# Performance work log

Measured on AMD Instinct MI355X. Metric: run time of the kernel, lower is better.

Reference implementation:

```python
import jax, jax.numpy as jnp
import numpy as np

L = 3
ALPHA = 1.0
BETA = 1.0
SCALING = 3.0
N_NODES = 100000
N_EDGES = 1250000
D_FEAT = 64


def spmm(row, col, w, z, n):
    # out[i] = sum_{e: row_e == i} w_e * z[col_e]  (torch_sparse.matmul reduce='sum')
    return jax.ops.segment_sum(z[col] * w[:, None], row, num_segments=n)


def setup_inputs() -> dict:
    key = jax.random.key(0)
    k1, k2, k3, k4 = jax.random.split(key, 4)
    x = jax.random.normal(k1, (N_NODES, D_FEAT), dtype=jnp.float32)
    edge_index = jax.random.randint(k2, (2, N_EDGES), 0, N_NODES, dtype=jnp.int64)
    # surrogate for symmetric-normalized adjacency weights
    edge_weight = jax.random.uniform(k3, (N_EDGES,), dtype=jnp.float32) * 0.2
    gammas = jnp.full((L + 1, 1), min(1.0 / SCALING, 1.0), dtype=jnp.float32)
    return {"x": x, "edge_index": edge_index, "edge_weight": edge_weight, "gammas": gammas}


def reference(x, edge_index, edge_weight, gammas):
    n = x.shape[0]
    row, col = edge_index[0], edge_index[1]
    a, b = ALPHA, BETA

    zs = [x]  # z_0 = x
    # l = 1: c * z0 + (a+b+2)/2 * A z0
    z1 = ((a - b) / 2) * zs[-1] + ((a + b + 2) / 2) * spmm(row, col, edge_weight, zs[-1], n)
    zs.append(z1)
    for l in range(2, L + 1):
        c0 = 2 * l * (l + a + b) * (2 * l + a + b - 2)
        c1 = (2 * l + a + b - 1) * (a ** 2 - b ** 2)
        c2 = (2 * l + a + b - 1) * (2 * l + a + b) * (2 * l + a + b - 2)
        c3 = 2 * (l + a - 1) * (l + b - 1) * (2 * l + a + b)
        Az = spmm(row, col, edge_weight, zs[-1], n)
        z = (c1 * zs[-1] + c2 * Az - c3 * zs[-2]) / c0
        zs.append(z)

    coefs = jnp.cumprod(jnp.tanh(gammas) * SCALING, axis=0)  # [L+1, 1]
    Z = jnp.stack(zs, axis=1)  # [N, L+1, d]
    return (Z * coefs).mean(axis=1)
```

## Files before the change

### kernel.cpp

```cpp
#include <hip/hip_runtime.h>
#include <hip/hip_fp16.h>
#include <math.h>

#define D 64
#define RB_SHIFT 6
#define RB 64
#define CAP 1024
#define CAPE 2048
#define MAX_NB 1600
#define LDSE 2048


__global__ void bin_scatter_kernel(const int* __restrict__ row, const int* __restrict__ col,
                                   const float* __restrict__ w,
                                   int* __restrict__ cursor,
                                   int2* __restrict__ binned, int E, int NB) {
    __shared__ int lbase[MAX_NB];
    __shared__ int lcur[MAX_NB];
    int chunk = (E + gridDim.x - 1) / gridDim.x;
    int lo = blockIdx.x * chunk;
    int hi = min(E, lo + chunk);
    for (int j = threadIdx.x; j < NB; j += blockDim.x) { lbase[j] = 0; lcur[j] = 0; }
    __syncthreads();
    for (int i = lo + threadIdx.x; i < hi; i += blockDim.x)
        atomicAdd(&lbase[row[i] >> RB_SHIFT], 1);
    __syncthreads();
    for (int j = threadIdx.x; j < NB; j += blockDim.x) {
        int c = lbase[j];
        int base = c ? atomicAdd(&cursor[j], c) : 0;
        lbase[j] = j * CAP + base;
    }
    __syncthreads();
    for (int i = lo + threadIdx.x; i < hi; i += blockDim.x) {
        int r = row[i];
        int b = r >> RB_SHIFT;
        int off = atomicAdd(&lcur[b], 1);
        binned[lbase[b] + off] = make_int2(col[i] | ((r & (RB - 1)) << 17), __float_as_int(w[i]));
    }
}

__global__ void bucket_sort_kernel(const int2* __restrict__ binned,
                                   const int* __restrict__ cursor,
                                   int2* __restrict__ edges, int2* __restrict__ rowinfo,
                                   int N, int NB) {
    __shared__ alignas(16) int2 perm[CAPE];
    __shared__ int hist[RB];
    __shared__ int plr[RB];
    __shared__ int scn[RB];
    __shared__ int pst[RB];
    __shared__ int cur[RB];
    int b = blockIdx.x, t = threadIdx.x;
    int base = b * CAP;
    int cnt = cursor[b];
    if (cnt > CAP) cnt = CAP;

    if (t < RB) hist[t] = 0;
    __syncthreads();
    for (int i = t; i < cnt; i += 256)
        atomicAdd(&hist[(binned[base + i].x >> 17) & (RB - 1)], 1);
    __syncthreads();
    if (t < RB) plr[t] = (hist[t] + 3) & ~3;
    __syncthreads();
    if (t < RB) {
        int qb = t & ~3;
        scn[t] = max(max(plr[qb], plr[qb | 1]), max(plr[qb | 2], plr[qb | 3]));
    }
    __syncthreads();
    for (int off = 1; off < RB; off <<= 1) {
        int v = (t < RB && t >= off) ? scn[t - off] : 0;
        __syncthreads();
        if (t < RB) scn[t] += v;
        __syncthreads();
    }
    if (t < RB) {
        int qb = t & ~3;
        int pl = max(max(plr[qb], plr[qb | 1]), max(plr[qb | 2], plr[qb | 3]));
        int ps = scn[t] - pl;
        pst[t] = ps;
        cur[t] = ps;
    }
    __syncthreads();
    for (int i = t; i < cnt; i += 256) {
        int2 e = binned[base + i];
        int rl = (e.x >> 17) & (RB - 1);
        int d = atomicAdd(&cur[rl], 1);
        __half2 wh2 = __half2half2(__float2half(__int_as_float(e.y)));
        perm[d] = make_int2((e.x & 0x1FFFF) << 7, *(int*)&wh2);
    }
    __syncthreads();
    if (t < RB) {
        int h = hist[t];
        int ps = pst[t];
        int qb = t & ~3;
        int pl = max(max(plr[qb], plr[qb | 1]), max(plr[qb | 2], plr[qb | 3]));
        int dummycol = (h > 0) ? perm[ps].x : 0;
        for (int i = h; i < pl; ++i) perm[ps + i] = make_int2(dummycol, 0);
        int r0 = b * RB + t;
        if (r0 < N) rowinfo[r0] = make_int2(b * CAPE + ps, pl);
    }
    __syncthreads();
    int ptotal = scn[RB - 1];
    if (ptotal > CAPE) ptotal = CAPE;
    int n4 = ptotal >> 1;
    const int4* ps4 = (const int4*)perm;
    int4* pd4 = (int4*)(edges + (size_t)b * CAPE);
    for (int i = t; i < n4; i += 256) pd4[i] = ps4[i];
}

__global__ void tohalf_kernel(const float4* __restrict__ in, ushort4* __restrict__ o, int n4) {
    int i = blockIdx.x * blockDim.x + threadIdx.x;
    int stride = gridDim.x * blockDim.x;
    for (; i < n4; i += stride) {
        float4 f = in[i];
        ushort4 h;
        h.x = __half_as_ushort(__float2half(f.x));
        h.y = __half_as_ushort(__float2half(f.y));
        h.z = __half_as_ushort(__float2half(f.z));
        h.w = __half_as_ushort(__float2half(f.w));
        o[i] = h;
    }
}

__device__ __forceinline__ void quad_row_acc_lds(const int2* __restrict__ lds_desc, int cnt,
                                                 const char* __restrict__ g2b, int boff,
                                                 __half2& acc0, __half2& acc1) {
    acc0 = __half2half2(__ushort_as_half((unsigned short)0));
    acc1 = acc0;
    for (int jb = 0; jb < cnt; jb += 4) {
        const int4* p4 = (const int4*)(lds_desc + jb);
        int4 d0 = p4[0];
        int4 d1 = p4[1];
        int2 g0 = *(const int2*)(g2b + (size_t)(unsigned)(d0.x + boff));
        int2 g1 = *(const int2*)(g2b + (size_t)(unsigned)(d0.z + boff));
        int2 g2 = *(const int2*)(g2b + (size_t)(unsigned)(d1.x + boff));
        int2 g3 = *(const int2*)(g2b + (size_t)(unsigned)(d1.z + boff));
        acc0 = __hfma2(*(__half2*)&d0.y, *(__half2*)&g0.x, acc0);
        acc1 = __hfma2(*(__half2*)&d0.y, *(__half2*)&g0.y, acc1);
        acc0 = __hfma2(*(__half2*)&d0.w, *(__half2*)&g1.x, acc0);
        acc1 = __hfma2(*(__half2*)&d0.w, *(__half2*)&g1.y, acc1);
        acc0 = __hfma2(*(__half2*)&d1.y, *(__half2*)&g2.x, acc0);
        acc1 = __hfma2(*(__half2*)&d1.y, *(__half2*)&g2.y, acc1);
        acc0 = __hfma2(*(__half2*)&d1.w, *(__half2*)&g3.x, acc0);
        acc1 = __hfma2(*(__half2*)&d1.w, *(__half2*)&g3.y, acc1);
    }
}

__global__ void spmm_z_kernel(const int2* __restrict__ rowinfo,
                              const int2* __restrict__ edges,
                              const __half2* __restrict__ gsrc2,
                              const __half2* __restrict__ zp2_2,
                              __half2* __restrict__ zdst2,
                              float cA, float cC, int N) {
    __shared__ alignas(16) int2 lds[LDSE];
    int t = threadIdx.x;
    int bid = blockIdx.x;
    int r0 = bid * 16;

    int gs = rowinfo[r0].x;
    int2 rlast = rowinfo[min(r0 + 15, N - 1)];
    int span = rlast.x + rlast.y - gs;
    if (span > LDSE) span = LDSE;
    {
        int n4 = span >> 1;
        const int4* s4 = (const int4*)(edges + gs);
        int4* d4 = (int4*)lds;
        for (int i = t; i < n4; i += 256) d4[i] = s4[i];
    }
    __syncthreads();

    int wv = t >> 6;
    int lane = t & 63;
    int q = lane >> 4;
    int k16 = lane & 15;
    int rr = r0 + wv * 4 + q;
    bool valid = rr < N;
    int r = valid ? rr : N - 1;

    int2 ri = rowinfo[r];
    int cnt = __builtin_amdgcn_readfirstlane(ri.y);
    int off = ri.x - gs;
    if (off < 0 || off + cnt > span) off = 0;

    int boff = k16 * 8;
    size_t rb = (size_t)r * 128 + boff;
    float2 p0 = make_float2(0.f, 0.f), p1 = p0;
    if (zp2_2) {
        int2 pz = *(const int2*)((const char*)zp2_2 + rb);
        p0 = __half22float2(*(__half2*)&pz.x);
        p1 = __half22float2(*(__half2*)&pz.y);
    }

    __half2 acc0, acc1;
    quad_row_acc_lds(lds + off, cnt, (const char*)gsrc2, boff, acc0, acc1);
    float2 a0 = __half22float2(acc0);
    float2 a1 = __half22float2(acc1);

    float2 z0 = make_float2(cA * a0.x, cA * a0.y);
    float2 z1 = make_float2(cA * a1.x, cA * a1.y);
    if (zp2_2) {
        z0.x = fmaf(cC, p0.x, z0.x); z0.y = fmaf(cC, p0.y, z0.y);
        z1.x = fmaf(cC, p1.x, z1.x); z1.y = fmaf(cC, p1.y, z1.y);
    }
    if (valid) {
        __half2 h0 = __floats2half2_rn(z0.x, z0.y);
        __half2 h1 = __floats2half2_rn(z1.x, z1.y);
        int2 st;
        st.x = *(int*)&h0;
        st.y = *(int*)&h1;
        *(int2*)((char*)zdst2 + rb) = st;
    }
}

__global__ void spmm_final_kernel(const int2* __restrict__ rowinfo,
                                  const int2* __restrict__ edges,
                                  const __half2* __restrict__ z2h2,
                                  const __half2* __restrict__ z1h2,
                                  const __half2* __restrict__ xh2,
                                  float* __restrict__ out,
                                  const float* __restrict__ gammas,
                                  float cA, float cC, int N) {
    __shared__ alignas(16) int2 lds[LDSE];
    int t = threadIdx.x;
    int bid = blockIdx.x;
    int r0 = bid * 16;

    int gs = rowinfo[r0].x;
    int2 rlast = rowinfo[min(r0 + 15, N - 1)];
    int span = rlast.x + rlast.y - gs;
    if (span > LDSE) span = LDSE;
    {
        int n4 = span >> 1;
        const int4* s4 = (const int4*)(edges + gs);
        int4* d4 = (int4*)lds;
        for (int i = t; i < n4; i += 256) d4[i] = s4[i];
    }
    __syncthreads();

    int wv = t >> 6;
    int lane = t & 63;
    int q = lane >> 4;
    int k16 = lane & 15;
    int rr = r0 + wv * 4 + q;
    bool valid = rr < N;
    int r = valid ? rr : N - 1;

    float t0 = tanhf(gammas[0]) * 3.0f;
    float t1 = t0 * (tanhf(gammas[1]) * 3.0f);
    float t2 = t1 * (tanhf(gammas[2]) * 3.0f);
    float t3 = t2 * (tanhf(gammas[3]) * 3.0f);

    int2 ri = rowinfo[r];
    int cnt = __builtin_amdgcn_readfirstlane(ri.y);
    int off = ri.x - gs;
    if (off < 0 || off + cnt > span) off = 0;

    int boff = k16 * 8;
    size_t rb = (size_t)r * 128 + boff;
    int2 pz1 = *(const int2*)((const char*)z1h2 + rb);
    int2 pz2 = *(const int2*)((const char*)z2h2 + rb);
    int2 pxv = *(const int2*)((const char*)xh2 + rb);

    __half2 acc0, acc1;
    quad_row_acc_lds(lds + off, cnt, (const char*)z2h2, boff, acc0, acc1);
    float2 a0 = __half22float2(acc0);
    float2 a1 = __half22float2(acc1);

    float2 z1v0 = __half22float2(*(__half2*)&pz1.x);
    float2 z1v1 = __half22float2(*(__half2*)&pz1.y);
    float2 z2v0 = __half22float2(*(__half2*)&pz2.x);
    float2 z2v1 = __half22float2(*(__half2*)&pz2.y);
    float2 xv0  = __half22float2(*(__half2*)&pxv.x);
    float2 xv1  = __half22float2(*(__half2*)&pxv.y);

    float2 z30 = make_float2(cA * a0.x + cC * z1v0.x, cA * a0.y + cC * z1v0.y);
    float2 z31 = make_float2(cA * a1.x + cC * z1v1.x, cA * a1.y + cC * z1v1.y);

    if (valid) {
        float4 o;
        o.x = 0.25f * (t0 * xv0.x + t1 * z1v0.x + t2 * z2v0.x + t3 * z30.x);
        o.y = 0.25f * (t0 * xv0.y + t1 * z1v0.y + t2 * z2v0.y + t3 * z30.y);
        o.z = 0.25f * (t0 * xv1.x + t1 * z1v1.x + t2 * z2v1.x + t3 * z31.x);
        o.w = 0.25f * (t0 * xv1.y + t1 * z1v1.y + t2 * z2v1.y + t3 * z31.y);
        ((float4*)out)[(size_t)r * 16 + k16] = o;
    }
}

extern "C" void kernel_launch(void* const* d_in, const int* in_sizes, int n_in,
                              void* d_out, int out_size, void* d_ws, size_t ws_size,
                              hipStream_t stream) {
    const float* x      = (const float*)d_in[0];
    const int*   ei     = (const int*)d_in[1];
    const float* w      = (const float*)d_in[2];
    const float* gammas = (const float*)d_in[3];

    const int E = in_sizes[1] / 2;
    const int N = in_sizes[0] / D;
    const long NF = (long)N * D;
    const int NB = (N + RB - 1) >> RB_SHIFT;

    float* out = (float*)d_out;

    char* p = (char*)d_ws;
    __half* xh  = (__half*)p;       p += NF * sizeof(__half);
    __half* z1h = (__half*)p;       p += NF * sizeof(__half);
    __half* z2h = (__half*)p;       p += NF * sizeof(__half);
    int* cursor = (int*)p;          p += NB * sizeof(int);
    p = (char*)(((uintptr_t)p + 15) & ~(uintptr_t)15);
    int2* rowinfo = (int2*)p;       p += (size_t)N * sizeof(int2);
    int2* binned = (int2*)p;        p += (size_t)NB * CAP * sizeof(int2);
    int2* edges = (int2*)p;

    const int* row = ei;
    const int* col = ei + E;

    const double a = 1.0, b = 1.0;
    const int blk = 256;

    hipMemsetAsync(cursor, 0, (size_t)NB * sizeof(int), stream);
    bin_scatter_kernel<<<256, 1024, 0, stream>>>(row, col, w, cursor, binned, E, NB);
    bucket_sort_kernel<<<NB, 256, 0, stream>>>(binned, cursor, edges, rowinfo, N, NB);
    tohalf_kernel<<<1024, blk, 0, stream>>>((const float4*)x, (ushort4*)xh, (int)(NF / 4));

    const int sgrid = (N + 15) / 16;

    {
        float cA = (float)((a + b + 2.0) / 2.0);
        spmm_z_kernel<<<sgrid, blk, 0, stream>>>(rowinfo, edges, (const __half2*)xh,
                                                 nullptr, (__half2*)z1h, cA, 0.0f, N);
    }

    {
        int l = 2;
        double c0 = 2.0 * l * (l + a + b) * (2.0 * l + a + b - 2.0);
        double c2 = (2.0 * l + a + b - 1.0) * (2.0 * l + a + b) * (2.0 * l + a + b - 2.0);
        double c3 = 2.0 * (l + a - 1.0) * (l + b - 1.0) * (2.0 * l + a + b);
        spmm_z_kernel<<<sgrid, blk, 0, stream>>>(rowinfo, edges, (const __half2*)z1h,
                                                 (const __half2*)xh, (__half2*)z2h,
                                                 (float)(c2 / c0), (float)(-c3 / c0), N);
    }

    {
        int l = 3;
        double c0 = 2.0 * l * (l + a + b) * (2.0 * l + a + b - 2.0);
        double c2 = (2.0 * l + a + b - 1.0) * (2.0 * l + a + b) * (2.0 * l + a + b - 2.0);
        double c3 = 2.0 * (l + a - 1.0) * (l + b - 1.0) * (2.0 * l + a + b);
        spmm_final_kernel<<<sgrid, blk, 0, stream>>>(rowinfo, edges, (const __half2*)z2h,
                                                     (const __half2*)z1h, (const __half2*)xh,
                                                     out, gammas,
                                                     (float)(c2 / c0), (float)(-c3 / c0), N);
    }
}
```

Before: 199.5 us.

## Replace bin-and-bucket-sort CSR build with row histogram, scan, and atomic scatter

The padded per-row edge layout used to be built in two stages: edges were binned into fixed-capacity buckets of 64 rows, then each bucket was sorted in shared memory and copied out. It is now built from a global per-row atomic histogram, a per-block scan that computes padded row offsets and fills pad slots, and a direct atomic scatter of edges into their final positions. This removes the intermediate binned buffer and the extra pass over it. In exchange it relies on two rounds of contended global atomics plus random 8-byte writes, and it adds a memset of a per-row counter array. Pad entries now point at column 0 with zero weight, and the order of edges within a row is no longer deterministic.

```diff
diff --git a/kernel.cpp b/kernel.cpp
--- a/kernel.cpp
+++ b/kernel.cpp
@@ -5,106 +5,85 @@
 #define D 64
 #define RB_SHIFT 6
 #define RB 64
-#define CAP 1024
 #define CAPE 2048
-#define MAX_NB 1600
 #define LDSE 2048
 
 
-__global__ void bin_scatter_kernel(const int* __restrict__ row, const int* __restrict__ col,
-                                   const float* __restrict__ w,
-                                   int* __restrict__ cursor,
-                                   int2* __restrict__ binned, int E, int NB) {
-    __shared__ int lbase[MAX_NB];
-    __shared__ int lcur[MAX_NB];
-    int chunk = (E + gridDim.x - 1) / gridDim.x;
-    int lo = blockIdx.x * chunk;
-    int hi = min(E, lo + chunk);
-    for (int j = threadIdx.x; j < NB; j += blockDim.x) { lbase[j] = 0; lcur[j] = 0; }
-    __syncthreads();
-    for (int i = lo + threadIdx.x; i < hi; i += blockDim.x)
-        atomicAdd(&lbase[row[i] >> RB_SHIFT], 1);
-    __syncthreads();
-    for (int j = threadIdx.x; j < NB; j += blockDim.x) {
-        int c = lbase[j];
-        int base = c ? atomicAdd(&cursor[j], c) : 0;
-        lbase[j] = j * CAP + base;
-    }
-    __syncthreads();
-    for (int i = lo + threadIdx.x; i < hi; i += blockDim.x) {
-        int r = row[i];
-        int b = r >> RB_SHIFT;
-        int off = atomicAdd(&lcur[b], 1);
-        binned[lbase[b] + off] = make_int2(col[i] | ((r & (RB - 1)) << 17), __float_as_int(w[i]));
-    }
-}
-
-__global__ void bucket_sort_kernel(const int2* __restrict__ binned,
-                                   const int* __restrict__ cursor,
-                                   int2* __restrict__ edges, int2* __restrict__ rowinfo,
-                                   int N, int NB) {
-    __shared__ alignas(16) int2 perm[CAPE];
-    __shared__ int hist[RB];
+__global__ void hist_kernel(const int* __restrict__ row, int* __restrict__ rowcnt, int E) {
+    int tid = blockIdx.x * blockDim.x + threadIdx.x;
+    int stride = gridDim.x * blockDim.x;
+    int n4 = E >> 2;
+    const int4* r4 = (const int4*)row;
+    for (int i = tid; i < n4; i += stride) {
+        int4 r = r4[i];
+        atomicAdd(&rowcnt[r.x], 1);
+        atomicAdd(&rowcnt[r.y], 1);
+        atomicAdd(&rowcnt[r.z], 1);
+        atomicAdd(&rowcnt[r.w], 1);
+    }
+    for (int i = (n4 << 2) + tid; i < E; i += stride)
+        atomicAdd(&rowcnt[row[i]], 1);
+}
+
+__global__ void scan_pad_kernel(const int* __restrict__ rowcnt,
+                                int2* __restrict__ edges,
+                                int2* __restrict__ rowinfo,
+                                int* __restrict__ curs, int N) {
     __shared__ int plr[RB];
     __shared__ int scn[RB];
-    __shared__ int pst[RB];
-    __shared__ int cur[RB];
     int b = blockIdx.x, t = threadIdx.x;
-    int base = b * CAP;
-    int cnt = cursor[b];
-    if (cnt > CAP) cnt = CAP;
-
-    if (t < RB) hist[t] = 0;
+    int r = b * RB + t;
+    int h = (r < N) ? rowcnt[r] : 0;
+    plr[t] = (h + 3) & ~3;
     __syncthreads();
-    for (int i = t; i < cnt; i += 256)
-        atomicAdd(&hist[(binned[base + i].x >> 17) & (RB - 1)], 1);
-    __syncthreads();
-    if (t < RB) plr[t] = (hist[t] + 3) & ~3;
-    __syncthreads();
-    if (t < RB) {
-        int qb = t & ~3;
-        scn[t] = max(max(plr[qb], plr[qb | 1]), max(plr[qb | 2], plr[qb | 3]));
-    }
+    int qb = t & ~3;
+    int pl = max(max(plr[qb], plr[qb | 1]), max(plr[qb | 2], plr[qb | 3]));
+    scn[t] = pl;
     __syncthreads();
     for (int off = 1; off < RB; off <<= 1) {
-        int v = (t < RB && t >= off) ? scn[t - off] : 0;
+        int v = (t >= off) ? scn[t - off] : 0;
         __syncthreads();
-        if (t < RB) scn[t] += v;
+        scn[t] += v;
         __syncthreads();
     }
-    if (t < RB) {
-        int qb = t & ~3;
-        int pl = max(max(plr[qb], plr[qb | 1]), max(plr[qb | 2], plr[qb | 3]));
-        int ps = scn[t] - pl;
-        pst[t] = ps;
-        cur[t] = ps;
-    }
-    __syncthreads();
-    for (int i = t; i < cnt; i += 256) {
-        int2 e = binned[base + i];
-        int rl = (e.x >> 17) & (RB - 1);
-        int d = atomicAdd(&cur[rl], 1);
-        __half2 wh2 = __half2half2(__float2half(__int_as_float(e.y)));
-        perm[d] = make_int2((e.x & 0x1FFFF) << 7, *(int*)&wh2);
-    }
-    __syncthreads();
-    if (t < RB) {
-        int h = hist[t];
-        int ps = pst[t];
-        int qb = t & ~3;
-        int pl = max(max(plr[qb], plr[qb | 1]), max(plr[qb | 2], plr[qb | 3]));
-        int dummycol = (h > 0) ? perm[ps].x : 0;
-        for (int i = h; i < pl; ++i) perm[ps + i] = make_int2(dummycol, 0);
-        int r0 = b * RB + t;
-        if (r0 < N) rowinfo[r0] = make_int2(b * CAPE + ps, pl);
-    }
-    __syncthreads();
-    int ptotal = scn[RB - 1];
-    if (ptotal > CAPE) ptotal = CAPE;
-    int n4 = ptotal >> 1;
-    const int4* ps4 = (const int4*)perm;
-    int4* pd4 = (int4*)(edges + (size_t)b * CAPE);
-    for (int i = t; i < n4; i += 256) pd4[i] = ps4[i];
+    int ps = scn[t] - pl;
+    if (ps + pl > CAPE) { ps = 0; pl = 0; h = 0; }
+    if (r < N) {
+        int start = b * CAPE + ps;
+        rowinfo[r] = make_int2(start, pl);
+        curs[r] = start;
+        for (int i = h; i < pl; ++i) edges[start + i] = make_int2(0, 0);
+    }
+}
+
+__global__ void scatter_kernel(const int* __restrict__ row, const int* __restrict__ col,
+                               const float* __restrict__ w,
+                               int* __restrict__ curs, int2* __restrict__ edges, int E) {
+    int tid = blockIdx.x * blockDim.x + threadIdx.x;
+    int stride = gridDim.x * blockDim.x;
+    int n4 = E >> 2;
+    const int4* r4 = (const int4*)row;
+    const int4* c4 = (const int4*)col;
+    const float4* w4 = (const float4*)w;
+    for (int i = tid; i < n4; i += stride) {
+        int4 rr = r4[i];
+        int4 cc = c4[i];
+        float4 ww = w4[i];
+        int rs[4] = {rr.x, rr.y, rr.z, rr.w};
+        int cs[4] = {cc.x, cc.y, cc.z, cc.w};
+        float wf[4] = {ww.x, ww.y, ww.z, ww.w};
+#pragma unroll
+        for (int q = 0; q < 4; ++q) {
+            int pos = atomicAdd(&curs[rs[q]], 1);
+            __half2 wh2 = __half2half2(__float2half(wf[q]));
+            edges[pos] = make_int2(cs[q] << 7, *(int*)&wh2);
+        }
+    }
+    for (int i = (n4 << 2) + tid; i < E; i += stride) {
+        int pos = atomicAdd(&curs[row[i]], 1);
+        __half2 wh2 = __half2half2(__float2half(w[i]));
+        edges[pos] = make_int2(col[i] << 7, *(int*)&wh2);
+    }
 }
 
 __global__ void tohalf_kernel(const float4* __restrict__ in, ushort4* __restrict__ o, int n4) {
@@ -304,10 +283,10 @@
     __half* xh  = (__half*)p;       p += NF * sizeof(__half);
     __half* z1h = (__half*)p;       p += NF * sizeof(__half);
     __half* z2h = (__half*)p;       p += NF * sizeof(__half);
-    int* cursor = (int*)p;          p += NB * sizeof(int);
+    int* rowcnt = (int*)p;          p += (size_t)N * sizeof(int);
+    int* curs   = (int*)p;          p += (size_t)N * sizeof(int);
     p = (char*)(((uintptr_t)p + 15) & ~(uintptr_t)15);
     int2* rowinfo = (int2*)p;       p += (size_t)N * sizeof(int2);
-    int2* binned = (int2*)p;        p += (size_t)NB * CAP * sizeof(int2);
     int2* edges = (int2*)p;
 
     const int* row = ei;
@@ -316,9 +295,10 @@
     const double a = 1.0, b = 1.0;
     const int blk = 256;
 
-    hipMemsetAsync(cursor, 0, (size_t)NB * sizeof(int), stream);
-    bin_scatter_kernel<<<256, 1024, 0, stream>>>(row, col, w, cursor, binned, E, NB);
-    bucket_sort_kernel<<<NB, 256, 0, stream>>>(binned, cursor, edges, rowinfo, N, NB);
+    hipMemsetAsync(rowcnt, 0, (size_t)N * sizeof(int), stream);
+    hist_kernel<<<1024, blk, 0, stream>>>(row, rowcnt, E);
+    scan_pad_kernel<<<NB, RB, 0, stream>>>(rowcnt, edges, rowinfo, curs, N);
+    scatter_kernel<<<1024, blk, 0, stream>>>(row, col, w, curs, edges, E);
     tohalf_kernel<<<1024, blk, 0, stream>>>((const float4*)x, (ushort4*)xh, (int)(NF / 4));
 
     const int sgrid = (N + 15) / 16;
```

Measured after the change: 316.4 us. +58.6%, slower.

## Fuse x-to-half conversion into binning and first SpMM into bucket sort

Applied to the files above, without the earlier changes.

Folds the fp32-to-fp16 conversion of x into the edge binning kernel, and has the bucket-sort kernel compute the first propagation (z1) straight from its LDS-resident sorted edges. This removes two kernel launches and the reload of edge descriptors from global memory for the first SpMM. In exchange the first SpMM runs with only NB blocks of 64 rows each, which lowers parallelism, and spmm_z_kernel now always reads a previous z.

```diff
diff --git a/kernel.cpp b/kernel.cpp
--- a/kernel.cpp
+++ b/kernel.cpp
@@ -11,10 +11,12 @@
 #define LDSE 2048
 
 
-__global__ void bin_scatter_kernel(const int* __restrict__ row, const int* __restrict__ col,
-                                   const float* __restrict__ w,
-                                   int* __restrict__ cursor,
-                                   int2* __restrict__ binned, int E, int NB) {
+__global__ void bin_scatter_tohalf_kernel(const int* __restrict__ row, const int* __restrict__ col,
+                                          const float* __restrict__ w,
+                                          int* __restrict__ cursor,
+                                          int2* __restrict__ binned, int E, int NB,
+                                          const float4* __restrict__ xin,
+                                          ushort4* __restrict__ xh4, int n4) {
     __shared__ int lbase[MAX_NB];
     __shared__ int lcur[MAX_NB];
     int chunk = (E + gridDim.x - 1) / gridDim.x;
@@ -37,87 +39,16 @@
         int off = atomicAdd(&lcur[b], 1);
         binned[lbase[b] + off] = make_int2(col[i] | ((r & (RB - 1)) << 17), __float_as_int(w[i]));
     }
-}
-
-__global__ void bucket_sort_kernel(const int2* __restrict__ binned,
-                                   const int* __restrict__ cursor,
-                                   int2* __restrict__ edges, int2* __restrict__ rowinfo,
-                                   int N, int NB) {
-    __shared__ alignas(16) int2 perm[CAPE];
-    __shared__ int hist[RB];
-    __shared__ int plr[RB];
-    __shared__ int scn[RB];
-    __shared__ int pst[RB];
-    __shared__ int cur[RB];
-    int b = blockIdx.x, t = threadIdx.x;
-    int base = b * CAP;
-    int cnt = cursor[b];
-    if (cnt > CAP) cnt = CAP;
-
-    if (t < RB) hist[t] = 0;
-    __syncthreads();
-    for (int i = t; i < cnt; i += 256)
-        atomicAdd(&hist[(binned[base + i].x >> 17) & (RB - 1)], 1);
-    __syncthreads();
-    if (t < RB) plr[t] = (hist[t] + 3) & ~3;
-    __syncthreads();
-    if (t < RB) {
-        int qb = t & ~3;
-        scn[t] = max(max(plr[qb], plr[qb | 1]), max(plr[qb | 2], plr[qb | 3]));
-    }
-    __syncthreads();
-    for (int off = 1; off < RB; off <<= 1) {
-        int v = (t < RB && t >= off) ? scn[t - off] : 0;
-        __syncthreads();
-        if (t < RB) scn[t] += v;
-        __syncthreads();
-    }
-    if (t < RB) {
-        int qb = t & ~3;
-        int pl = max(max(plr[qb], plr[qb | 1]), max(plr[qb | 2], plr[qb | 3]));
-        int ps = scn[t] - pl;
-        pst[t] = ps;
-        cur[t] = ps;
-    }
-    __syncthreads();
-    for (int i = t; i < cnt; i += 256) {
-        int2 e = binned[base + i];
-        int rl = (e.x >> 17) & (RB - 1);
-        int d = atomicAdd(&cur[rl], 1);
-        __half2 wh2 = __half2half2(__float2half(__int_as_float(e.y)));
-        perm[d] = make_int2((e.x & 0x1FFFF) << 7, *(int*)&wh2);
-    }
-    __syncthreads();
-    if (t < RB) {
-        int h = hist[t];
-        int ps = pst[t];
-        int qb = t & ~3;
-        int pl = max(max(plr[qb], plr[qb | 1]), max(plr[qb | 2], plr[qb | 3]));
-        int dummycol = (h > 0) ? perm[ps].x : 0;
-        for (int i = h; i < pl; ++i) perm[ps + i] = make_int2(dummycol, 0);
-        int r0 = b * RB + t;
-        if (r0 < N) rowinfo[r0] = make_int2(b * CAPE + ps, pl);
-    }
-    __syncthreads();
-    int ptotal = scn[RB - 1];
-    if (ptotal > CAPE) ptotal = CAPE;
-    int n4 = ptotal >> 1;
-    const int4* ps4 = (const int4*)perm;
-    int4* pd4 = (int4*)(edges + (size_t)b * CAPE);
-    for (int i = t; i < n4; i += 256) pd4[i] = ps4[i];
-}
-
-__global__ void tohalf_kernel(const float4* __restrict__ in, ushort4* __restrict__ o, int n4) {
-    int i = blockIdx.x * blockDim.x + threadIdx.x;
-    int stride = gridDim.x * blockDim.x;
-    for (; i < n4; i += stride) {
-        float4 f = in[i];
+    int gtid = blockIdx.x * blockDim.x + threadIdx.x;
+    int gstride = gridDim.x * blockDim.x;
+    for (int i = gtid; i < n4; i += gstride) {
+        float4 f = xin[i];
         ushort4 h;
         h.x = __half_as_ushort(__float2half(f.x));
         h.y = __half_as_ushort(__float2half(f.y));
         h.z = __half_as_ushort(__float2half(f.z));
         h.w = __half_as_ushort(__float2half(f.w));
-        o[i] = h;
+        xh4[i] = h;
     }
 }
 
@@ -145,6 +76,104 @@
     }
 }
 
+__global__ void bucket_sort_spmm1_kernel(const int2* __restrict__ binned,
+                                         const int* __restrict__ cursor,
+                                         int2* __restrict__ edges, int2* __restrict__ rowinfo,
+                                         const __half2* __restrict__ xh2,
+                                         __half2* __restrict__ z1h2,
+                                         float cA, int N, int NB) {
+    __shared__ alignas(16) int2 perm[CAPE];
+    __shared__ int hist[RB];
+    __shared__ int plr[RB];
+    __shared__ int scn[RB];
+    __shared__ int pst[RB];
+    __shared__ int cur[RB];
+    __shared__ int plc[RB];
+    int b = blockIdx.x, t = threadIdx.x;
+    int base = b * CAP;
+    int cnt = cursor[b];
+    if (cnt > CAP) cnt = CAP;
+
+    if (t < RB) hist[t] = 0;
+    __syncthreads();
+    for (int i = t; i < cnt; i += 256)
+        atomicAdd(&hist[(binned[base + i].x >> 17) & (RB - 1)], 1);
+    __syncthreads();
+    if (t < RB) plr[t] = (hist[t] + 3) & ~3;
+    __syncthreads();
+    if (t < RB) {
+        int qb = t & ~3;
+        scn[t] = max(max(plr[qb], plr[qb | 1]), max(plr[qb | 2], plr[qb | 3]));
+    }
+    __syncthreads();
+    for (int off = 1; off < RB; off <<= 1) {
+        int v = (t < RB && t >= off) ? scn[t - off] : 0;
+        __syncthreads();
+        if (t < RB) scn[t] += v;
+        __syncthreads();
+    }
+    if (t < RB) {
+        int qb = t & ~3;
+        int pl = max(max(plr[qb], plr[qb | 1]), max(plr[qb | 2], plr[qb | 3]));
+        int ps = scn[t] - pl;
+        pst[t] = ps;
+        cur[t] = ps;
+        plc[t] = pl;
+    }
+    __syncthreads();
+    for (int i = t; i < cnt; i += 256) {
+        int2 e = binned[base + i];
+        int rl = (e.x >> 17) & (RB - 1);
+        int d = atomicAdd(&cur[rl], 1);
+        __half2 wh2 = __half2half2(__float2half(__int_as_float(e.y)));
+        perm[d] = make_int2((e.x & 0x1FFFF) << 7, *(int*)&wh2);
+    }
+    __syncthreads();
+    if (t < RB) {
+        int h = hist[t];
+        int ps = pst[t];
+        int pl = plc[t];
+        int dummycol = (h > 0) ? perm[ps].x : 0;
+        for (int i = h; i < pl; ++i) perm[ps + i] = make_int2(dummycol, 0);
+        int r0 = b * RB + t;
+        if (r0 < N) rowinfo[r0] = make_int2(b * CAPE + ps, pl);
+    }
+    __syncthreads();
+    {
+        int ptotal = scn[RB - 1];
+        if (ptotal > CAPE) ptotal = CAPE;
+        int n4 = ptotal >> 1;
+        const int4* ps4 = (const int4*)perm;
+        int4* pd4 = (int4*)(edges + (size_t)b * CAPE);
+        for (int i = t; i < n4; i += 256) pd4[i] = ps4[i];
+    }
+
+    int w = t >> 6;
+    int lane = t & 63;
+    int q = lane >> 4;
+    int k16 = lane & 15;
+    int boff = k16 * 8;
+    for (int p = 0; p < 4; ++p) {
+        int qi = p * 4 + w;
+        int lr = qi * 4 + q;
+        int r = b * RB + lr;
+        int ccnt = __builtin_amdgcn_readfirstlane(plc[qi * 4]);
+        int off = pst[lr];
+        __half2 acc0, acc1;
+        quad_row_acc_lds(perm + off, ccnt, (const char*)xh2, boff, acc0, acc1);
+        float2 a0 = __half22float2(acc0);
+        float2 a1 = __half22float2(acc1);
+        if (r < N) {
+            __half2 h0 = __floats2half2_rn(cA * a0.x, cA * a0.y);
+            __half2 h1 = __floats2half2_rn(cA * a1.x, cA * a1.y);
+            int2 st;
+            st.x = *(int*)&h0;
+            st.y = *(int*)&h1;
+            *(int2*)((char*)z1h2 + (size_t)r * 128 + boff) = st;
+        }
+    }
+}
+
 __global__ void spmm_z_kernel(const int2* __restrict__ rowinfo,
                               const int2* __restrict__ edges,
                               const __half2* __restrict__ gsrc2,
@@ -183,24 +212,17 @@
 
     int boff = k16 * 8;
     size_t rb = (size_t)r * 128 + boff;
-    float2 p0 = make_float2(0.f, 0.f), p1 = p0;
-    if (zp2_2) {
-        int2 pz = *(const int2*)((const char*)zp2_2 + rb);
-        p0 = __half22float2(*(__half2*)&pz.x);
-        p1 = __half22float2(*(__half2*)&pz.y);
-    }
+    int2 pz = *(const int2*)((const char*)zp2_2 + rb);
+    float2 p0 = __half22float2(*(__half2*)&pz.x);
+    float2 p1 = __half22float2(*(__half2*)&pz.y);
 
     __half2 acc0, acc1;
     quad_row_acc_lds(lds + off, cnt, (const char*)gsrc2, boff, acc0, acc1);
     float2 a0 = __half22float2(acc0);
     float2 a1 = __half22float2(acc1);
 
-    float2 z0 = make_float2(cA * a0.x, cA * a0.y);
-    float2 z1 = make_float2(cA * a1.x, cA * a1.y);
-    if (zp2_2) {
-        z0.x = fmaf(cC, p0.x, z0.x); z0.y = fmaf(cC, p0.y, z0.y);
-        z1.x = fmaf(cC, p1.x, z1.x); z1.y = fmaf(cC, p1.y, z1.y);
-    }
+    float2 z0 = make_float2(fmaf(cC, p0.x, cA * a0.x), fmaf(cC, p0.y, cA * a0.y));
+    float2 z1 = make_float2(fmaf(cC, p1.x, cA * a1.x), fmaf(cC, p1.y, cA * a1.y));
     if (valid) {
         __half2 h0 = __floats2half2_rn(z0.x, z0.y);
         __half2 h1 = __floats2half2_rn(z1.x, z1.y);
@@ -317,17 +339,18 @@
     const int blk = 256;
 
     hipMemsetAsync(cursor, 0, (size_t)NB * sizeof(int), stream);
-    bin_scatter_kernel<<<256, 1024, 0, stream>>>(row, col, w, cursor, binned, E, NB);
-    bucket_sort_kernel<<<NB, 256, 0, stream>>>(binned, cursor, edges, rowinfo, N, NB);
-    tohalf_kernel<<<1024, blk, 0, stream>>>((const float4*)x, (ushort4*)xh, (int)(NF / 4));
+    bin_scatter_tohalf_kernel<<<256, 1024, 0, stream>>>(row, col, w, cursor, binned, E, NB,
+                                                        (const float4*)x, (ushort4*)xh,
+                                                        (int)(NF / 4));
+
+    {
+        float cA = (float)((a + b + 2.0) / 2.0);
+        bucket_sort_spmm1_kernel<<<NB, blk, 0, stream>>>(binned, cursor, edges, rowinfo,
+                                                         (const __half2*)xh, (__half2*)z1h,
+                                                         cA, N, NB);
+    }
 
     const int sgrid = (N + 15) / 16;
-
-    {
-        float cA = (float)((a + b + 2.0) / 2.0);
-        spmm_z_kernel<<<sgrid, blk, 0, stream>>>(rowinfo, edges, (const __half2*)xh,
-                                                 nullptr, (__half2*)z1h, cA, 0.0f, N);
-    }
 
     {
         int l = 2;
```

New measurement: 195.2 us. 2.2% less time.
